# Optimization experiments

Hardware: AMD Instinct MI355X
Metric: run time of the kernel (lower is better)

## Reference

```python
import jax, jax.numpy as jnp
import numpy as np

COMMITMENT_COST = 0.25


def setup_inputs() -> dict:
    key = jax.random.key(0)
    k1, k2 = jax.random.split(key)
    B, H, W, D = 64, 64, 64, 64
    K = 1024
    inputs = jax.random.normal(k1, (B, H, W, D), dtype=jnp.float32)
    # codebook initialized ~ N(0, 1/sqrt(D)) as in the torch module
    codebook = jax.random.normal(k2, (K, D), dtype=jnp.float32) / jnp.sqrt(jnp.float32(D))
    return {"inputs": inputs, "codebook": codebook}


def reference(inputs, codebook):
    K, D = codebook.shape
    input_shape = inputs.shape
    flat = inputs.reshape(-1, D)                      # (N, D)
    N = flat.shape[0]
    distances = (
        jnp.sum(flat * flat, axis=1, keepdims=True)
        + jnp.sum(codebook * codebook, axis=1)
        - 2.0 * jnp.matmul(flat, codebook.T)
    )
    encoding_indices = jnp.argmin(distances, axis=1)  # (N,)
    # gather instead of one-hot @ codebook (same math, no N x K one-hot)
    quantized = codebook[encoding_indices].reshape(input_shape)
    # straight-through estimator
    quantized_st = inputs + jax.lax.stop_gradient(quantized - inputs)
    e_latent_loss = jnp.mean((jax.lax.stop_gradient(quantized_st) - inputs) ** 2)
    q_latent_loss = jnp.mean((quantized - jax.lax.stop_gradient(inputs)) ** 2)
    commitment_loss = COMMITMENT_COST * e_latent_loss
    codebook_loss = q_latent_loss
    vq_loss = commitment_loss + codebook_loss
    # perplexity of codebook usage (avg one-hot probs via scatter-add)
    counts = jnp.zeros((K,), dtype=jnp.float32).at[encoding_indices].add(1.0)
    avg_probs = counts / jnp.float32(N)
    perplexity = jnp.exp(-jnp.sum(avg_probs * jnp.log(avg_probs + 1e-10)))
    tokens = encoding_indices.reshape(input_shape[:-1])
    return quantized_st, tokens, vq_loss, commitment_loss, codebook_loss, perplexity
```

## Files before the change

### kernel.cpp

```cpp
#include <hip/hip_runtime.h>
#include <hip/hip_bf16.h>
#include <math.h>

#define D 64
#define K 1024
#define N_VEC 262144
#define FLAG_CAP 65536
#define T_BIAS 144.0f
#define CLAMP_HI 159.99998474121094f
#define ULP128 1.52587890625e-5f
#define FLAG_THR (41u << 10)

typedef __attribute__((ext_vector_type(8))) short short8v;
typedef __attribute__((ext_vector_type(4))) float f32x4;

__device__ __forceinline__ unsigned short f2bf_rne(float f) {
  unsigned u = __builtin_bit_cast(unsigned, f);
  u += 0x7FFFu + ((u >> 16) & 1u);
  return (unsigned short)(u >> 16);
}
__device__ __forceinline__ float bf2f(unsigned short h) {
  unsigned u = ((unsigned)h) << 16;
  return __builtin_bit_cast(float, u);
}


__global__ __launch_bounds__(256) void vq_prep_kernel(
    const float* __restrict__ cb, float* __restrict__ cnorm,
    float* __restrict__ hcn, unsigned short* __restrict__ pk,
    float* __restrict__ cbT, int write_t) {
  int k = blockIdx.x * 256 + threadIdx.x;
  if (k >= K) return;
  const float4* cp = reinterpret_cast<const float4*>(cb + (size_t)k * D);
  unsigned short* row = pk + (size_t)k * 128;
  float s = 0.f;
#pragma unroll
  for (int j4 = 0; j4 < 16; ++j4) {
    float4 v = cp[j4];
    float ff[4] = {v.x, v.y, v.z, v.w};
    ushort4 hh, ll;
    unsigned short* hp = (unsigned short*)&hh;
    unsigned short* lp = (unsigned short*)&ll;
#pragma unroll
    for (int u = 0; u < 4; ++u) {
      float f = ff[u];
      s = fmaf(f, f, s);
      unsigned short hb = f2bf_rne(f);
      float lo = f - bf2f(hb);
      hp[u] = hb;
      lp[u] = f2bf_rne(lo);
      if (write_t) cbT[(size_t)(j4 * 4 + u) * K + k] = f;
    }
    reinterpret_cast<ushort4*>(row)[j4] = hh;
    reinterpret_cast<ushort4*>(row + 64)[j4] = ll;
  }
  cnorm[k] = s;
  hcn[k] = -0.5f * s;
}

__device__ __forceinline__ float block_reduce_sum_256(float v) {
#pragma unroll
  for (int o = 32; o > 0; o >>= 1) v += __shfl_down(v, o, 64);
  __shared__ float s[4];
  int lane = threadIdx.x & 63;
  int w = threadIdx.x >> 6;
  if (lane == 0) s[w] = v;
  __syncthreads();
  float r = 0.f;
  if (threadIdx.x == 0) r = s[0] + s[1] + s[2] + s[3];
  return r;
}

__global__ __launch_bounds__(256) void vq_argmin_mfma_kernel(
    const float* __restrict__ x, const unsigned short* __restrict__ pk,
    const float* __restrict__ hcn, float* __restrict__ tok_out,
    unsigned int* __restrict__ counts, float* __restrict__ sq_accum,
    unsigned int* __restrict__ flag_cnt, unsigned int* __restrict__ flag_list) {
  __shared__ unsigned int hist[K];
  for (int i = threadIdx.x; i < K; i += 256) hist[i] = 0u;
  __syncthreads();

  const int lane = threadIdx.x & 63;
  const int w = threadIdx.x >> 6;
  const int c16 = lane & 15;
  const int g4 = lane >> 4;
  const int wave_base = blockIdx.x * 256 + w * 64;

  short8v ah[4][2], al[4][2];
  float xx[4];
#pragma unroll
  for (int rt = 0; rt < 4; ++rt) {
    float xp = 0.f;
#pragma unroll
    for (int s = 0; s < 2; ++s) {
      int row = wave_base + rt * 16 + c16;
      const float* p = x + (size_t)row * D + s * 32 + g4 * 8;
      float4 f0 = *(const float4*)(p);
      float4 f1 = *(const float4*)(p + 4);
      float ff[8] = {f0.x, f0.y, f0.z, f0.w, f1.x, f1.y, f1.z, f1.w};
      short8v h, l;
#pragma unroll
      for (int j = 0; j < 8; ++j) {
        xp = fmaf(ff[j], ff[j], xp);
        unsigned short hb = f2bf_rne(ff[j]);
        float lo = ff[j] - bf2f(hb);
        h[j] = (short)hb;
        l[j] = (short)f2bf_rne(lo);
      }
      ah[rt][s] = h;
      al[rt][s] = l;
    }
    float t1 = xp + __shfl_xor(xp, 16, 64);
    xx[rt] = t1 + __shfl_xor(t1, 32, 64);
  }

  unsigned bP[4][4], b2P[4][4];
#pragma unroll
  for (int rt = 0; rt < 4; ++rt)
#pragma unroll
    for (int r = 0; r < 4; ++r) {
      bP[rt][r] = 0u;
      b2P[rt][r] = 0u;
    }

  const unsigned short* pbase = pk + (size_t)c16 * 128 + (size_t)g4 * 8;

  short8v cb0 = *(const short8v*)(pbase);
  short8v cb1 = *(const short8v*)(pbase + 32);
  short8v cb2 = *(const short8v*)(pbase + 64);
  short8v cb3 = *(const short8v*)(pbase + 96);
  float hcur = hcn[c16];

  for (int t = 0; t < 64; ++t) {
    int tn = (t < 63) ? (t + 1) : 63;
    const unsigned short* pn = pbase + (size_t)tn * 2048;
    short8v nb0 = *(const short8v*)(pn);
    short8v nb1 = *(const short8v*)(pn + 32);
    short8v nb2 = *(const short8v*)(pn + 64);
    short8v nb3 = *(const short8v*)(pn + 96);
    float hnext = hcn[tn * 16 + c16];

    f32x4 cinit = {hcur, hcur, hcur, hcur};
    f32x4 zro = {0.f, 0.f, 0.f, 0.f};
    const unsigned pcv = 1023u - (unsigned)(t * 16 + c16);
#pragma unroll
    for (int rt = 0; rt < 4; ++rt) {
      f32x4 a0 = cinit;
      f32x4 a1 = zro;
      a0 = __builtin_amdgcn_mfma_f32_16x16x32_bf16(ah[rt][0], cb0, a0, 0, 0, 0);
      a1 = __builtin_amdgcn_mfma_f32_16x16x32_bf16(ah[rt][1], cb1, a1, 0, 0, 0);
      a0 = __builtin_amdgcn_mfma_f32_16x16x32_bf16(ah[rt][0], cb2, a0, 0, 0, 0);
      a1 = __builtin_amdgcn_mfma_f32_16x16x32_bf16(ah[rt][1], cb3, a1, 0, 0, 0);
      a0 = __builtin_amdgcn_mfma_f32_16x16x32_bf16(al[rt][0], cb0, a0, 0, 0, 0);
      a1 = __builtin_amdgcn_mfma_f32_16x16x32_bf16(al[rt][1], cb1, a1, 0, 0, 0);
#pragma unroll
      for (int r = 0; r < 4; ++r) {
        float T = a0[r] + a1[r];
        float Tb = T + T_BIAS;
        Tb = __builtin_amdgcn_fmed3f(Tb, 128.0f, CLAMP_HI);
        unsigned bits = __builtin_bit_cast(unsigned, Tb);
        unsigned p = (bits << 10) | pcv;
        unsigned mn = p < bP[rt][r] ? p : bP[rt][r];
        bP[rt][r] = p > bP[rt][r] ? p : bP[rt][r];
        b2P[rt][r] = mn > b2P[rt][r] ? mn : b2P[rt][r];
      }
    }
    cb0 = nb0; cb1 = nb1; cb2 = nb2; cb3 = nb3; hcur = hnext;
  }

  float sqloc = 0.f;
#pragma unroll
  for (int rt = 0; rt < 4; ++rt) {
#pragma unroll
    for (int r = 0; r < 4; ++r) {
      unsigned b = bP[rt][r], b2 = b2P[rt][r];
#pragma unroll
      for (int m = 1; m < 16; m <<= 1) {
        unsigned ob = (unsigned)__shfl_xor((int)b, m, 64);
        unsigned ob2 = (unsigned)__shfl_xor((int)b2, m, 64);
        unsigned mn = b < ob ? b : ob;
        b = b > ob ? b : ob;
        unsigned t2 = b2 > ob2 ? b2 : ob2;
        b2 = t2 > mn ? t2 : mn;
      }
      float xxr = __shfl(xx[rt], g4 * 4 + r, 64);
      if (c16 == 0) {
        int code = 1023 - (int)(b & 1023u);
        int grow = wave_base + rt * 16 + g4 * 4 + r;
        tok_out[grow] = (float)code;
        atomicAdd(&hist[code], 1u);
        float Tt = 128.0f + (float)(b >> 10) * ULP128;
        sqloc += (xxr + 2.0f * T_BIAS) - 2.0f * Tt;
        if (b - b2 < FLAG_THR) {
          unsigned pfl = atomicAdd(flag_cnt, 1u);
          if (pfl < FLAG_CAP) flag_list[pfl] = (unsigned)grow;
        }
      }
    }
  }
  __syncthreads();
  for (int i = threadIdx.x; i < K; i += 256) {
    unsigned h = hist[i];
    if (h) atomicAdd(&counts[i], h);
  }
  float bs = block_reduce_sum_256(sqloc);
  if (threadIdx.x == 0) atomicAdd(sq_accum, bs);
}

__global__ __launch_bounds__(256) void vq_cleanup_blk_kernel(
    const float* __restrict__ x, const float* __restrict__ cbT,
    const float* __restrict__ cnorm, float* __restrict__ tok,
    unsigned int* __restrict__ counts, float* __restrict__ sq_accum,
    const unsigned int* __restrict__ flag_cnt,
    const unsigned int* __restrict__ flag_list) {
  __shared__ float xs[D];
  __shared__ float wb[4], wd[4];
  __shared__ int wk[4];
  unsigned nf = *flag_cnt;
  if (nf > FLAG_CAP) nf = FLAG_CAP;
  const int t = threadIdx.x;
  for (unsigned f = blockIdx.x; f < nf; f += gridDim.x) {
    int vid = (int)flag_list[f];
    int old = (int)tok[vid];
    __syncthreads();
    if (t < D) xs[t] = x[(size_t)vid * D + t];
    __syncthreads();

    float xx = 0.f;
#pragma unroll
    for (int j = 0; j < D; ++j) xx = fmaf(xs[j], xs[j], xx);

    float d0 = 0.f, d1 = 0.f, d2 = 0.f, d3 = 0.f;
#pragma unroll 8
    for (int j = 0; j < D; ++j) {
      float xj = xs[j];
      const float* row = cbT + (size_t)j * K + t;
      d0 = fmaf(xj, row[0], d0);
      d1 = fmaf(xj, row[256], d1);
      d2 = fmaf(xj, row[512], d2);
      d3 = fmaf(xj, row[768], d3);
    }
    float dist0 = (xx + cnorm[t]) - 2.0f * d0;
    float dist1 = (xx + cnorm[t + 256]) - 2.0f * d1;
    float dist2 = (xx + cnorm[t + 512]) - 2.0f * d2;
    float dist3 = (xx + cnorm[t + 768]) - 2.0f * d3;

    float dold = 3.4e38f;
    if ((old & 255) == t) {
      int slot = old >> 8;
      dold = slot == 0 ? dist0 : slot == 1 ? dist1 : slot == 2 ? dist2 : dist3;
    }

    float best = dist0;
    int bk = t;
    if (dist1 < best) { best = dist1; bk = t + 256; }
    if (dist2 < best) { best = dist2; bk = t + 512; }
    if (dist3 < best) { best = dist3; bk = t + 768; }

#pragma unroll
    for (int m = 1; m < 64; m <<= 1) {
      float ob = __shfl_xor(best, m, 64);
      int oi = __shfl_xor(bk, m, 64);
      bool take = (ob < best) || (ob == best && oi < bk);
      best = take ? ob : best;
      bk = take ? oi : bk;
      dold = fminf(dold, __shfl_xor(dold, m, 64));
    }
    if ((t & 63) == 0) { wb[t >> 6] = best; wk[t >> 6] = bk; wd[t >> 6] = dold; }
    __syncthreads();
    if (t == 0) {
#pragma unroll
      for (int wv = 1; wv < 4; ++wv) {
        bool take = (wb[wv] < best) || (wb[wv] == best && wk[wv] < bk);
        best = take ? wb[wv] : best;
        bk = take ? wk[wv] : bk;
        dold = fminf(dold, wd[wv]);
      }
      if (bk != old) {
        tok[vid] = (float)bk;
        atomicAdd(&counts[old], 0xFFFFFFFFu);
        atomicAdd(&counts[bk], 1u);
        atomicAdd(sq_accum, best - dold);
      }
    }
  }
}

__global__ __launch_bounds__(256) void vq_cleanup_kernel(
    const float* __restrict__ x, const float* __restrict__ cb,
    const float* __restrict__ cnorm, float* __restrict__ tok,
    unsigned int* __restrict__ counts, float* __restrict__ sq_accum,
    const unsigned int* __restrict__ flag_cnt,
    const unsigned int* __restrict__ flag_list) {
  const int lane = threadIdx.x & 63;
  const int gw = blockIdx.x * (blockDim.x >> 6) + (threadIdx.x >> 6);
  const int nw = gridDim.x * (blockDim.x >> 6);
  unsigned nf = *flag_cnt;
  if (nf > FLAG_CAP) nf = FLAG_CAP;
  for (unsigned f = gw; f < nf; f += nw) {
    int vid = (int)flag_list[f];
    int old = (int)tok[vid];
    const float* xv = x + (size_t)vid * D;
    float xr[D];
#pragma unroll
    for (int j = 0; j < 16; ++j) {
      float4 v = ((const float4*)xv)[j];
      xr[4 * j] = v.x; xr[4 * j + 1] = v.y;
      xr[4 * j + 2] = v.z; xr[4 * j + 3] = v.w;
    }
    float xx = 0.f;
#pragma unroll
    for (int j = 0; j < D; ++j) xx = fmaf(xr[j], xr[j], xx);
    float best = 3.4e38f, dold = 3.4e38f;
    int bidx = K;
    for (int i = 0; i < 16; ++i) {
      int k = i * 64 + lane;
      const float* c = cb + (size_t)k * D;
      float acc = 0.f;
#pragma unroll
      for (int j = 0; j < D; ++j) acc = fmaf(xr[j], c[j], acc);
      float dist = (xx + cnorm[k]) - 2.0f * acc;
      if (dist < best) { best = dist; bidx = k; }
      if (k == old) dold = dist;
    }
#pragma unroll
    for (int m = 1; m < 64; m <<= 1) {
      float ob = __shfl_xor(best, m, 64);
      int oi = __shfl_xor(bidx, m, 64);
      bool take = (ob < best) || (ob == best && oi < bidx);
      best = take ? ob : best;
      bidx = take ? oi : bidx;
      dold = fminf(dold, __shfl_xor(dold, m, 64));
    }
    if (lane == 0 && bidx != old) {
      tok[vid] = (float)bidx;
      atomicAdd(&counts[old], 0xFFFFFFFFu);
      atomicAdd(&counts[bidx], 1u);
      atomicAdd(sq_accum, best - dold);
    }
  }
}

__global__ __launch_bounds__(256) void vq_writeq_kernel(
    const float* __restrict__ cb, const float* __restrict__ tok,
    float* __restrict__ outq) {
  const int total4 = N_VEC * (D / 4);
  for (int idx4 = blockIdx.x * 256 + threadIdx.x; idx4 < total4;
       idx4 += gridDim.x * 256) {
    int vid = idx4 >> 4;
    int j4 = idx4 & 15;
    int t = (int)tok[vid];
    reinterpret_cast<float4*>(outq)[idx4] =
        reinterpret_cast<const float4*>(cb)[t * 16 + j4];
  }
}

__global__ __launch_bounds__(256) void vq_finalize_kernel(
    const unsigned int* __restrict__ counts, const float* __restrict__ sq_accum,
    float* __restrict__ out_scalars) {
  float h = 0.f;
  for (int i = threadIdx.x; i < K; i += 256) {
    float p = (float)counts[i] / (float)N_VEC;
    h -= p * logf(p + 1e-10f);
  }
  float hs = block_reduce_sum_256(h);
  if (threadIdx.x == 0) {
    float m = sq_accum[0] / (float)((size_t)N_VEC * D);
    out_scalars[0] = 1.25f * m;
    out_scalars[1] = 0.25f * m;
    out_scalars[2] = m;
    out_scalars[3] = expf(hs);
  }
}

extern "C" void kernel_launch(void* const* d_in, const int* in_sizes, int n_in,
                              void* d_out, int out_size, void* d_ws,
                              size_t ws_size, hipStream_t stream) {
  const float* x = (const float*)d_in[0];
  const float* cb = (const float*)d_in[1];

  float* outq = (float*)d_out;
  float* tok = outq + (size_t)N_VEC * D;
  float* scal = tok + N_VEC;

  unsigned int* counts = (unsigned int*)d_ws;
  float* sq = (float*)d_ws + K;
  unsigned int* flag_cnt = (unsigned int*)d_ws + K + 1;
  float* cnorm = (float*)d_ws + K + 4;
  float* hcn = (float*)d_ws + 2 * K + 4;
  unsigned int* flag_list = (unsigned int*)d_ws + 3 * K + 4;
  size_t base_dw = (size_t)3 * K + 4 + FLAG_CAP;
  unsigned short* pk = (unsigned short*)((unsigned int*)d_ws + base_dw);
  size_t pk_dw = (size_t)K * 128 / 2;
  float* cbT = (float*)((unsigned int*)d_ws + base_dw + pk_dw);
  size_t need_t = (base_dw + pk_dw + (size_t)K * D) * 4;
  int use_t = (ws_size >= need_t) ? 1 : 0;

  hipMemsetAsync(d_ws, 0, (size_t)(K + 2) * sizeof(float), stream);

  vq_prep_kernel<<<(K + 255) / 256, 256, 0, stream>>>(cb, cnorm, hcn, pk, cbT,
                                                      use_t);
  vq_argmin_mfma_kernel<<<N_VEC / 256, 256, 0, stream>>>(
      x, pk, hcn, tok, counts, sq, flag_cnt, flag_list);
  if (use_t) {
    vq_cleanup_blk_kernel<<<2048, 256, 0, stream>>>(x, cbT, cnorm, tok, counts,
                                                    sq, flag_cnt, flag_list);
  } else {
    vq_cleanup_kernel<<<1024, 256, 0, stream>>>(x, cb, cnorm, tok, counts, sq,
                                                flag_cnt, flag_list);
  }
  vq_writeq_kernel<<<4096, 256, 0, stream>>>(cb, tok, outq);
  vq_finalize_kernel<<<1, 256, 0, stream>>>(counts, sq, scal);
}
```

Measured before the change: 214.5 us.

## Fuse quantized output write into argmin and cleanup kernels, fold bias into norms

Removes the separate gather kernel that wrote the quantized output. The argmin kernel now writes each row's codebook vector directly, and the cleanup kernels rewrite rows whose token changed. The T_BIAS offset is folded into the precomputed half-norms, saving an add per distance element, and the near-tie flag threshold is widened. This avoids an extra full pass reading tokens and the codebook plus one launch. In exchange the argmin epilogue issues more stores, and more rows may be sent to cleanup.

```diff
diff --git a/kernel.cpp b/kernel.cpp
--- a/kernel.cpp
+++ b/kernel.cpp
@@ -9,7 +9,7 @@
 #define T_BIAS 144.0f
 #define CLAMP_HI 159.99998474121094f
 #define ULP128 1.52587890625e-5f
-#define FLAG_THR (41u << 10)
+#define FLAG_THR (164u << 10)
 
 typedef __attribute__((ext_vector_type(8))) short short8v;
 typedef __attribute__((ext_vector_type(4))) float f32x4;
@@ -55,7 +55,7 @@
     reinterpret_cast<ushort4*>(row + 64)[j4] = ll;
   }
   cnorm[k] = s;
-  hcn[k] = -0.5f * s;
+  hcn[k] = T_BIAS - 0.5f * s;
 }
 
 __device__ __forceinline__ float block_reduce_sum_256(float v) {
@@ -72,8 +72,9 @@
 }
 
 __global__ __launch_bounds__(256) void vq_argmin_mfma_kernel(
-    const float* __restrict__ x, const unsigned short* __restrict__ pk,
-    const float* __restrict__ hcn, float* __restrict__ tok_out,
+    const float* __restrict__ x, const float* __restrict__ cb,
+    const unsigned short* __restrict__ pk, const float* __restrict__ hcn,
+    float* __restrict__ tok_out, float* __restrict__ outq,
     unsigned int* __restrict__ counts, float* __restrict__ sq_accum,
     unsigned int* __restrict__ flag_cnt, unsigned int* __restrict__ flag_list) {
   __shared__ unsigned int hist[K];
@@ -156,8 +157,7 @@
 #pragma unroll
       for (int r = 0; r < 4; ++r) {
         float T = a0[r] + a1[r];
-        float Tb = T + T_BIAS;
-        Tb = __builtin_amdgcn_fmed3f(Tb, 128.0f, CLAMP_HI);
+        float Tb = __builtin_amdgcn_fmed3f(T, 128.0f, CLAMP_HI);
         unsigned bits = __builtin_bit_cast(unsigned, Tb);
         unsigned p = (bits << 10) | pcv;
         unsigned mn = p < bP[rt][r] ? p : bP[rt][r];
@@ -183,10 +183,12 @@
         unsigned t2 = b2 > ob2 ? b2 : ob2;
         b2 = t2 > mn ? t2 : mn;
       }
+      int code = 1023 - (int)(b & 1023u);
+      int grow = wave_base + rt * 16 + g4 * 4 + r;
+      reinterpret_cast<float4*>(outq)[(size_t)grow * 16 + c16] =
+          reinterpret_cast<const float4*>(cb)[code * 16 + c16];
       float xxr = __shfl(xx[rt], g4 * 4 + r, 64);
       if (c16 == 0) {
-        int code = 1023 - (int)(b & 1023u);
-        int grow = wave_base + rt * 16 + g4 * 4 + r;
         tok_out[grow] = (float)code;
         atomicAdd(&hist[code], 1u);
         float Tt = 128.0f + (float)(b >> 10) * ULP128;
@@ -208,14 +210,16 @@
 }
 
 __global__ __launch_bounds__(256) void vq_cleanup_blk_kernel(
-    const float* __restrict__ x, const float* __restrict__ cbT,
-    const float* __restrict__ cnorm, float* __restrict__ tok,
+    const float* __restrict__ x, const float* __restrict__ cb,
+    const float* __restrict__ cbT, const float* __restrict__ cnorm,
+    float* __restrict__ tok, float* __restrict__ outq,
     unsigned int* __restrict__ counts, float* __restrict__ sq_accum,
     const unsigned int* __restrict__ flag_cnt,
     const unsigned int* __restrict__ flag_list) {
   __shared__ float xs[D];
   __shared__ float wb[4], wd[4];
   __shared__ int wk[4];
+  __shared__ int s_new;
   unsigned nf = *flag_cnt;
   if (nf > FLAG_CAP) nf = FLAG_CAP;
   const int t = threadIdx.x;
@@ -276,21 +280,27 @@
         bk = take ? wk[wv] : bk;
         dold = fminf(dold, wd[wv]);
       }
+      s_new = -1;
       if (bk != old) {
+        s_new = bk;
         tok[vid] = (float)bk;
         atomicAdd(&counts[old], 0xFFFFFFFFu);
         atomicAdd(&counts[bk], 1u);
         atomicAdd(sq_accum, best - dold);
       }
     }
+    __syncthreads();
+    int nk = s_new;
+    if (nk >= 0 && t < D)
+      outq[(size_t)vid * D + t] = cb[(size_t)nk * D + t];
   }
 }
 
 __global__ __launch_bounds__(256) void vq_cleanup_kernel(
     const float* __restrict__ x, const float* __restrict__ cb,
     const float* __restrict__ cnorm, float* __restrict__ tok,
-    unsigned int* __restrict__ counts, float* __restrict__ sq_accum,
-    const unsigned int* __restrict__ flag_cnt,
+    float* __restrict__ outq, unsigned int* __restrict__ counts,
+    float* __restrict__ sq_accum, const unsigned int* __restrict__ flag_cnt,
     const unsigned int* __restrict__ flag_list) {
   const int lane = threadIdx.x & 63;
   const int gw = blockIdx.x * (blockDim.x >> 6) + (threadIdx.x >> 6);
@@ -332,26 +342,15 @@
       bidx = take ? oi : bidx;
       dold = fminf(dold, __shfl_xor(dold, m, 64));
     }
-    if (lane == 0 && bidx != old) {
-      tok[vid] = (float)bidx;
-      atomicAdd(&counts[old], 0xFFFFFFFFu);
-      atomicAdd(&counts[bidx], 1u);
-      atomicAdd(sq_accum, best - dold);
-    }
-  }
-}
-
-__global__ __launch_bounds__(256) void vq_writeq_kernel(
-    const float* __restrict__ cb, const float* __restrict__ tok,
-    float* __restrict__ outq) {
-  const int total4 = N_VEC * (D / 4);
-  for (int idx4 = blockIdx.x * 256 + threadIdx.x; idx4 < total4;
-       idx4 += gridDim.x * 256) {
-    int vid = idx4 >> 4;
-    int j4 = idx4 & 15;
-    int t = (int)tok[vid];
-    reinterpret_cast<float4*>(outq)[idx4] =
-        reinterpret_cast<const float4*>(cb)[t * 16 + j4];
+    if (bidx != old) {
+      if (lane == 0) {
+        tok[vid] = (float)bidx;
+        atomicAdd(&counts[old], 0xFFFFFFFFu);
+        atomicAdd(&counts[bidx], 1u);
+        atomicAdd(sq_accum, best - dold);
+      }
+      outq[(size_t)vid * D + lane] = cb[(size_t)bidx * D + lane];
+    }
   }
 }
 
@@ -401,14 +400,14 @@
   vq_prep_kernel<<<(K + 255) / 256, 256, 0, stream>>>(cb, cnorm, hcn, pk, cbT,
                                                       use_t);
   vq_argmin_mfma_kernel<<<N_VEC / 256, 256, 0, stream>>>(
-      x, pk, hcn, tok, counts, sq, flag_cnt, flag_list);
+      x, cb, pk, hcn, tok, outq, counts, sq, flag_cnt, flag_list);
   if (use_t) {
-    vq_cleanup_blk_kernel<<<2048, 256, 0, stream>>>(x, cbT, cnorm, tok, counts,
-                                                    sq, flag_cnt, flag_list);
+    vq_cleanup_blk_kernel<<<2048, 256, 0, stream>>>(
+        x, cb, cbT, cnorm, tok, outq, counts, sq, flag_cnt, flag_list);
   } else {
-    vq_cleanup_kernel<<<1024, 256, 0, stream>>>(x, cb, cnorm, tok, counts, sq,
-                                                flag_cnt, flag_list);
-  }
-  vq_writeq_kernel<<<4096, 256, 0, stream>>>(cb, tok, outq);
+    vq_cleanup_kernel<<<1024, 256, 0, stream>>>(x, cb, cnorm, tok, outq,
+                                                counts, sq, flag_cnt,
+                                                flag_list);
+  }
   vq_finalize_kernel<<<1, 256, 0, stream>>>(counts, sq, scal);
 }
```

Result: slower. 241.0 us (+12.3%).
